# Kernel tuning notes

Hardware: AMD Instinct MI355X
Metric: run time of the kernel (lower is better)

Reference implementation:

```python
import jax, jax.numpy as jnp
import numpy as np


def _skew(p):
    # p: (...,3) -> (...,3,3) skew-symmetric matrices
    x, y, z = p[..., 0], p[..., 1], p[..., 2]
    o = jnp.zeros_like(x)
    return jnp.stack([
        jnp.stack([o, -z, y], -1),
        jnp.stack([z, o, -x], -1),
        jnp.stack([-y, x, o], -1)], -2)


def _so3exp(w):
    # Rodrigues formula for a single (3,) rotation vector
    theta = jnp.linalg.norm(w)
    small = theta < 1e-7
    th = jnp.where(small, 1.0, theta)
    W = _skew(w)
    A = jnp.where(small, 1.0, jnp.sin(th) / th)
    B = jnp.where(small, 0.5, (1.0 - jnp.cos(th)) / (th * th))
    return jnp.eye(3, dtype=w.dtype) + A * W + B * (W @ W)


def setup_inputs() -> dict:
    key = jax.random.key(0)
    k1, k2, k3, k4, k5, k6 = jax.random.split(key, 6)
    N, C, H, W = 100000, 128, 480, 640
    xy = jax.random.uniform(k1, (N, 2), minval=-1.0, maxval=1.0)
    z = jax.random.uniform(k2, (N, 1), minval=4.0, maxval=8.0)
    pts3D = jnp.concatenate([xy, z], -1).astype(jnp.float32)
    feature_ref = jax.random.normal(k3, (N, C), dtype=jnp.float32)
    feature_map_query = jax.random.normal(k4, (C, H, W), dtype=jnp.float32)
    feature_grad_x = jax.random.normal(k5, (C, H, W), dtype=jnp.float32) * 0.1
    feature_grad_y = jax.random.normal(k6, (C, H, W), dtype=jnp.float32) * 0.1
    K = jnp.array([[400.0, 0.0, 320.0], [0.0, 400.0, 200.0], [0.0, 0.0, 1.0]], dtype=jnp.float32)
    return {"pts3D": pts3D, "feature_ref": feature_ref,
            "feature_map_query": feature_map_query,
            "feature_grad_x": feature_grad_x, "feature_grad_y": feature_grad_y,
            "K": K, "n_iters": 5}


def reference(pts3D, feature_ref, feature_map_query, feature_grad_x, feature_grad_y, K, n_iters):
    C, H, W = feature_map_query.shape
    N = pts3D.shape[0]

    def gather(fm, ii, jj):
        return fm[:, ii, jj].T  # (N, C)

    def project(Rm, tv):
        p = pts3D @ Rm.T + tv                       # (N,3) points in camera frame
        uv = p @ K.T
        proj = jnp.round(uv[:, :2] / uv[:, 2:3]).astype(jnp.int32) - 1  # (N,2) [x,y]
        ii = jnp.clip(proj[:, 1], 0, H - 1)          # row (flip)
        jj = jnp.clip(proj[:, 0], 0, W - 1)          # col
        return p, ii, jj

    def step(carry, i):
        R, t, lam, lr, prev_cost = carry
        p, ii, jj = project(R, t)
        error = gather(feature_map_query, ii, jj) - feature_ref  # (N,C)
        cost_mean = (0.5 * (error ** 2).sum(-1)).mean()
        prev_cost = jnp.where(i == 0, cost_mean, prev_cost)
        eye = jnp.broadcast_to(jnp.eye(3, dtype=p.dtype), (N, 3, 3))
        J_p_T = jnp.concatenate([eye, -_skew(p)], -1)            # (N,3,6)
        fx, fy = K[0, 0], K[1, 1]
        x, y, z = p[:, 0], p[:, 1], p[:, 2]
        o = jnp.ones_like(z); zz = jnp.zeros_like(z)
        J_px_p = jnp.stack([fx * o, zz, -fx * x / z, zz, fy * o, -fy * y / z], -1)
        J_px_p = J_px_p.reshape(N, 2, 3) / z[:, None, None]       # (N,2,3)
        gx = gather(feature_grad_x, ii, jj)
        gy = gather(feature_grad_y, ii, jj)
        J_f_px = jnp.stack([gx, gy], -1)                          # (N,C,2)
        J = jnp.einsum('ncp,npq,nqk->nck', J_f_px, J_px_p, J_p_T)  # (N,C,6)
        g = jnp.einsum('nck,nc->k', J, error)                     # (6,)
        Hess = jnp.einsum('nci,ncj->ij', J, J)                    # (6,6)
        Hd = Hess + jnp.diag(jnp.diagonal(Hess) + 1e-9) * lam     # LM damping
        delta = -lr * jnp.linalg.solve(Hd, g)
        dt, dw = delta[:3], delta[3:6]
        dR = _so3exp(dw)
        R_new = dR @ R
        t_new = dR @ t + dt
        _, ii2, jj2 = project(R_new, t_new)
        new_error = gather(feature_map_query, ii2, jj2) - feature_ref
        new_cost = (0.5 * (new_error ** 2).sum(-1)).mean()
        worse = new_cost > prev_cost
        lam = jnp.clip(lam * jnp.where(worse, 10.0, 0.1), 1e-6, 1e4)
        lr = jnp.where(worse, jnp.clip(0.1 * lr, 1e-3, 1.0), 0.1)
        R = jnp.where(worse, R, R_new)
        t = jnp.where(worse, t, t_new)
        prev_cost = jnp.where(worse, prev_cost, new_cost)
        return (R, t, lam, lr, prev_cost), None

    R0 = jnp.eye(3, dtype=pts3D.dtype)
    t0 = jnp.array([1.0, 1.0, 0.0], dtype=pts3D.dtype)
    init = (R0, t0, jnp.float32(0.01), jnp.float32(0.1), jnp.float32(0.0))
    (R, t, _, _, _), _ = jax.lax.scan(step, init, jnp.arange(n_iters))
    return R, t
```

## Files before the change

### kernel.cpp

```cpp
#include <hip/hip_runtime.h>

#define NPTS 100000
#define CCH  128
#define HIMG 480
#define WIMG 640
#define HWSZ (HIMG*WIMG)
#define TROW 384

struct State {
  double accA[28];
  double accC[28];
  double accB;
  double prev_cost;
  float R[9];
  float t[3];
  float Rc[9];
  float tc[3];
  float lam;
  float lr;
};

__device__ State g_st;

__device__ __forceinline__ float sel6(int k, float a0,float a1,float a2,float a3,float a4,float a5){
  float r = a0;
  r = (k==1)?a1:r; r = (k==2)?a2:r; r = (k==3)?a3:r; r = (k==4)?a4:r; r = (k==5)?a5:r;
  return r;
}

__global__ void k_init(){
  if(threadIdx.x==0){
    for(int i=0;i<28;i++){ g_st.accA[i]=0.0; g_st.accC[i]=0.0; }
    g_st.accB=0.0; g_st.prev_cost=0.0;
    g_st.R[0]=1.f; g_st.R[1]=0.f; g_st.R[2]=0.f;
    g_st.R[3]=0.f; g_st.R[4]=1.f; g_st.R[5]=0.f;
    g_st.R[6]=0.f; g_st.R[7]=0.f; g_st.R[8]=1.f;
    g_st.t[0]=1.f; g_st.t[1]=1.f; g_st.t[2]=0.f;
    g_st.lam=0.01f; g_st.lr=0.1f;
  }
}

#define TIDX(c,p) ((c)*66 + ((p) ^ ((((c)>>5)&3)<<4)))

__global__ __launch_bounds__(256) void k_transpose(
    const float* __restrict__ Q, const float* __restrict__ GX,
    const float* __restrict__ GY, float* __restrict__ T)
{
  __shared__ float tile[128*66];
  const int pbase = blockIdx.x * 64;
  const int t = threadIdx.x;

  for(int m=0;m<3;m++){
    const float* __restrict__ src = (m==0)?Q:((m==1)?GX:GY);
    __syncthreads();
    #pragma unroll
    for(int k=0;k<8;k++){
      const int c = (t>>4) + 16*k;
      const float4 v = *reinterpret_cast<const float4*>(src + (size_t)c*HWSZ + pbase + ((t&15)<<2));
      float* d = &tile[TIDX(c, (t&15)<<2)];
      d[0]=v.x; d[1]=v.y; d[2]=v.z; d[3]=v.w;
    }
    __syncthreads();
    const int p  = t>>2;
    const int cb = (t&3)*32;
    float4* dst = reinterpret_cast<float4*>(T + (size_t)(pbase+p)*TROW + m*128 + cb);
    #pragma unroll
    for(int k=0;k<8;k++){
      float4 v;
      v.x = tile[TIDX(cb+4*k+0, p)];
      v.y = tile[TIDX(cb+4*k+1, p)];
      v.z = tile[TIDX(cb+4*k+2, p)];
      v.w = tile[TIDX(cb+4*k+3, p)];
      dst[k] = v;
    }
  }
}

__global__ __launch_bounds__(256) void k_pass(
    const float* __restrict__ pts, const float* __restrict__ ref,
    const float* __restrict__ T,   const float* __restrict__ Kin, int cand)
{
  __shared__ double wacc[4][28];
  const int lane = threadIdx.x & 63;
  const int wid  = threadIdx.x >> 6;

  const float fx=Kin[0], cx=Kin[2], fy=Kin[4], cy=Kin[5];
  const float* Rp = cand ? g_st.Rc : g_st.R;
  const float* tp = cand ? g_st.tc : g_st.t;
  const float R00=Rp[0],R01=Rp[1],R02=Rp[2];
  const float R10=Rp[3],R11=Rp[4],R12=Rp[5];
  const float R20=Rp[6],R21=Rp[7],R22=Rp[8];
  const float t0=tp[0],t1=tp[1],t2=tp[2];

  int role = 3, ci = 0, cj = 0;
  if(lane < 6){ role = 0; ci = lane; cj = lane; }
  else if(lane < 27){
    role = 1;
    const int tt = lane - 6;
    int i = 5;
    i = (tt < 20) ? 4 : i;
    i = (tt < 18) ? 3 : i;
    i = (tt < 15) ? 2 : i;
    i = (tt < 11) ? 1 : i;
    i = (tt <  6) ? 0 : i;
    const int rs = (i==0)?0:(i==1)?6:(i==2)?11:(i==3)?15:(i==4)?18:20;
    ci = i; cj = i + (tt - rs);
  }
  else if(lane == 27){ role = 2; }

  double acc = 0.0;
  const int c0 = lane*2;
  const int wstride = gridDim.x*4;
  for(int n = blockIdx.x*4 + wid; n < NPTS; n += wstride){
    const float X=pts[3*n], Y=pts[3*n+1], Z=pts[3*n+2];
    const float x = R00*X + R01*Y + R02*Z + t0;
    const float y = R10*X + R11*Y + R12*Z + t1;
    const float z = R20*X + R21*Y + R22*Z + t2;
    const float uu = fx*x + cx*z;
    const float vv = fy*y + cy*z;
    const int pjx = (int)rintf(uu/z) - 1;
    const int pjy = (int)rintf(vv/z) - 1;
    const int jj = pjx<0?0:(pjx>(WIMG-1)?(WIMG-1):pjx);
    const int ii = pjy<0?0:(pjy>(HIMG-1)?(HIMG-1):pjy);
    const int idx = ii*WIMG + jj;

    const float* base = T + (size_t)idx*TROW + c0;
    const float2 qq = *reinterpret_cast<const float2*>(base);
    const float2 gg = *reinterpret_cast<const float2*>(base + 128);
    const float2 hh = *reinterpret_cast<const float2*>(base + 256);
    const float2 rr = *reinterpret_cast<const float2*>(ref + n*CCH + c0);
    const float e0 = qq.x-rr.x, e1 = qq.y-rr.y;

    float see = e0*e0 + e1*e1;
    float sb1 = gg.x*e0 + gg.y*e1;
    float sb2 = hh.x*e0 + hh.y*e1;
    float sa11= gg.x*gg.x + gg.y*gg.y;
    float sa12= gg.x*hh.x + gg.y*hh.y;
    float sa22= hh.x*hh.x + hh.y*hh.y;
    #pragma unroll
    for(int m=1;m<64;m<<=1){
      see += __shfl_xor(see,m);
      sb1 += __shfl_xor(sb1,m);
      sb2 += __shfl_xor(sb2,m);
      sa11+= __shfl_xor(sa11,m);
      sa12+= __shfl_xor(sa12,m);
      sa22+= __shfl_xor(sa22,m);
    }

    const float iz = 1.0f/z;
    const float ux = x*iz, vy = y*iz;
    const float m00=fx*iz, m01=0.f,    m02=-fx*ux*iz, m03=-fx*ux*vy,       m04=fx*(1.f+ux*ux), m05=-fx*vy;
    const float m10=0.f,   m11=fy*iz,  m12=-fy*vy*iz, m13=-fy*(1.f+vy*vy), m14=fy*ux*vy,       m15=fy*ux;

    float contrib;
    if(role==0){
      const float M0=sel6(ci,m00,m01,m02,m03,m04,m05);
      const float M1=sel6(ci,m10,m11,m12,m13,m14,m15);
      contrib = M0*sb1 + M1*sb2;
    } else if(role==1){
      const float M0i=sel6(ci,m00,m01,m02,m03,m04,m05);
      const float M1i=sel6(ci,m10,m11,m12,m13,m14,m15);
      const float M0j=sel6(cj,m00,m01,m02,m03,m04,m05);
      const float M1j=sel6(cj,m10,m11,m12,m13,m14,m15);
      contrib = sa11*(M0i*M0j) + sa12*(M0i*M1j + M1i*M0j) + sa22*(M1i*M1j);
    } else if(role==2){
      contrib = see;
    } else {
      contrib = 0.f;
    }
    acc += (double)contrib;
  }

  if(lane<28) wacc[wid][lane] = acc;
  __syncthreads();
  if(threadIdx.x<28){
    double s = wacc[0][threadIdx.x]+wacc[1][threadIdx.x]+wacc[2][threadIdx.x]+wacc[3][threadIdx.x];
    atomicAdd(cand ? &g_st.accC[threadIdx.x] : &g_st.accA[threadIdx.x], s);
  }
}

__global__ void k_update2(){
  if(threadIdx.x!=0) return;
  const double new_cost = 0.5*g_st.accC[27]/(double)NPTS;
  const bool worse = new_cost > g_st.prev_cost;
  float lam = g_st.lam * (worse?10.0f:0.1f);
  g_st.lam = fminf(fmaxf(lam,1e-6f),10000.0f);
  g_st.lr  = worse ? fminf(fmaxf(0.1f*g_st.lr,0.001f),1.0f) : 0.1f;
  if(!worse){
    for(int i=0;i<28;i++) g_st.accA[i]=g_st.accC[i];
    for(int i=0;i<9;i++) g_st.R[i]=g_st.Rc[i];
    for(int i=0;i<3;i++) g_st.t[i]=g_st.tc[i];
    g_st.prev_cost = new_cost;
  }
  for(int i=0;i<28;i++) g_st.accC[i]=0.0;
}

__global__ __launch_bounds__(256) void k_accum(
    const float* __restrict__ pts, const float* __restrict__ ref,
    const float* __restrict__ Q,   const float* __restrict__ GX,
    const float* __restrict__ GY,  const float* __restrict__ Kin)
{
  __shared__ double wacc[4][28];
  const int lane = threadIdx.x & 63;
  const int wid  = threadIdx.x >> 6;

  const float fx=Kin[0], cx=Kin[2], fy=Kin[4], cy=Kin[5];
  const float R00=g_st.R[0],R01=g_st.R[1],R02=g_st.R[2];
  const float R10=g_st.R[3],R11=g_st.R[4],R12=g_st.R[5];
  const float R20=g_st.R[6],R21=g_st.R[7],R22=g_st.R[8];
  const float t0=g_st.t[0],t1=g_st.t[1],t2=g_st.t[2];

  int role = 3, ci = 0, cj = 0;
  if(lane < 6){ role = 0; ci = lane; cj = lane; }
  else if(lane < 27){
    role = 1;
    const int tt = lane - 6;
    int i = 5;
    i = (tt < 20) ? 4 : i;
    i = (tt < 18) ? 3 : i;
    i = (tt < 15) ? 2 : i;
    i = (tt < 11) ? 1 : i;
    i = (tt <  6) ? 0 : i;
    const int rs = (i==0)?0:(i==1)?6:(i==2)?11:(i==3)?15:(i==4)?18:20;
    ci = i; cj = i + (tt - rs);
  }
  else if(lane == 27){ role = 2; }

  double acc = 0.0;
  const int c0 = lane*2;
  const int wstride = gridDim.x*4;
  for(int n = blockIdx.x*4 + wid; n < NPTS; n += wstride){
    const float X=pts[3*n], Y=pts[3*n+1], Z=pts[3*n+2];
    const float x = R00*X + R01*Y + R02*Z + t0;
    const float y = R10*X + R11*Y + R12*Z + t1;
    const float z = R20*X + R21*Y + R22*Z + t2;
    const float uu = fx*x + cx*z;
    const float vv = fy*y + cy*z;
    const int pjx = (int)rintf(uu/z) - 1;
    const int pjy = (int)rintf(vv/z) - 1;
    const int jj = pjx<0?0:(pjx>(WIMG-1)?(WIMG-1):pjx);
    const int ii = pjy<0?0:(pjy>(HIMG-1)?(HIMG-1):pjy);
    const int idx = ii*WIMG + jj;

    const int o0 = c0*HWSZ + idx;
    const float q0 = Q[o0],  q1 = Q[o0+HWSZ];
    const float gx0= GX[o0], gx1= GX[o0+HWSZ];
    const float gy0= GY[o0], gy1= GY[o0+HWSZ];
    const float2 rr = *reinterpret_cast<const float2*>(ref + n*CCH + c0);
    const float e0 = q0-rr.x, e1 = q1-rr.y;

    float see = e0*e0 + e1*e1;
    float sb1 = gx0*e0 + gx1*e1;
    float sb2 = gy0*e0 + gy1*e1;
    float sa11= gx0*gx0 + gx1*gx1;
    float sa12= gx0*gy0 + gx1*gy1;
    float sa22= gy0*gy0 + gy1*gy1;
    #pragma unroll
    for(int m=1;m<64;m<<=1){
      see += __shfl_xor(see,m);
      sb1 += __shfl_xor(sb1,m);
      sb2 += __shfl_xor(sb2,m);
      sa11+= __shfl_xor(sa11,m);
      sa12+= __shfl_xor(sa12,m);
      sa22+= __shfl_xor(sa22,m);
    }

    const float iz = 1.0f/z;
    const float ux = x*iz, vy = y*iz;
    const float m00=fx*iz, m01=0.f,    m02=-fx*ux*iz, m03=-fx*ux*vy,       m04=fx*(1.f+ux*ux), m05=-fx*vy;
    const float m10=0.f,   m11=fy*iz,  m12=-fy*vy*iz, m13=-fy*(1.f+vy*vy), m14=fy*ux*vy,       m15=fy*ux;

    float contrib;
    if(role==0){
      const float M0=sel6(ci,m00,m01,m02,m03,m04,m05);
      const float M1=sel6(ci,m10,m11,m12,m13,m14,m15);
      contrib = M0*sb1 + M1*sb2;
    } else if(role==1){
      const float M0i=sel6(ci,m00,m01,m02,m03,m04,m05);
      const float M1i=sel6(ci,m10,m11,m12,m13,m14,m15);
      const float M0j=sel6(cj,m00,m01,m02,m03,m04,m05);
      const float M1j=sel6(cj,m10,m11,m12,m13,m14,m15);
      contrib = sa11*(M0i*M0j) + sa12*(M0i*M1j + M1i*M0j) + sa22*(M1i*M1j);
    } else if(role==2){
      contrib = see;
    } else {
      contrib = 0.f;
    }
    acc += (double)contrib;
  }

  if(lane<28) wacc[wid][lane] = acc;
  __syncthreads();
  if(threadIdx.x<28){
    double s = wacc[0][threadIdx.x]+wacc[1][threadIdx.x]+wacc[2][threadIdx.x]+wacc[3][threadIdx.x];
    atomicAdd(&g_st.accA[threadIdx.x], s);
  }
}

__global__ __launch_bounds__(256) void k_cost(
    const float* __restrict__ pts, const float* __restrict__ ref,
    const float* __restrict__ Q,   const float* __restrict__ Kin)
{
  __shared__ double wacc[4];
  const int lane = threadIdx.x & 63;
  const int wid  = threadIdx.x >> 6;

  const float fx=Kin[0], cx=Kin[2], fy=Kin[4], cy=Kin[5];
  const float R00=g_st.Rc[0],R01=g_st.Rc[1],R02=g_st.Rc[2];
  const float R10=g_st.Rc[3],R11=g_st.Rc[4],R12=g_st.Rc[5];
  const float R20=g_st.Rc[6],R21=g_st.Rc[7],R22=g_st.Rc[8];
  const float t0=g_st.tc[0],t1=g_st.tc[1],t2=g_st.tc[2];

  double acc = 0.0;
  const int c0 = lane*2;
  const int wstride = gridDim.x*4;
  for(int n = blockIdx.x*4 + wid; n < NPTS; n += wstride){
    const float X=pts[3*n], Y=pts[3*n+1], Z=pts[3*n+2];
    const float x = R00*X + R01*Y + R02*Z + t0;
    const float y = R10*X + R11*Y + R12*Z + t1;
    const float z = R20*X + R21*Y + R22*Z + t2;
    const float uu = fx*x + cx*z;
    const float vv = fy*y + cy*z;
    const int pjx = (int)rintf(uu/z) - 1;
    const int pjy = (int)rintf(vv/z) - 1;
    const int jj = pjx<0?0:(pjx>(WIMG-1)?(WIMG-1):pjx);
    const int ii = pjy<0?0:(pjy>(HIMG-1)?(HIMG-1):pjy);
    const int idx = ii*WIMG + jj;

    const int o0 = c0*HWSZ + idx;
    const float q0 = Q[o0], q1 = Q[o0+HWSZ];
    const float2 rr = *reinterpret_cast<const float2*>(ref + n*CCH + c0);
    const float e0 = q0-rr.x, e1 = q1-rr.y;
    float see = e0*e0 + e1*e1;
    #pragma unroll
    for(int m=1;m<64;m<<=1) see += __shfl_xor(see,m);
    if(lane==0) acc += (double)see;
  }
  if(lane==0) wacc[wid]=acc;
  __syncthreads();
  if(threadIdx.x==0) atomicAdd(&g_st.accB, wacc[0]+wacc[1]+wacc[2]+wacc[3]);
}

__global__ void k_solve(int iter){
  if(threadIdx.x!=0) return;
  const double cost_mean = 0.5*g_st.accA[27]/(double)NPTS;
  if(iter==0) g_st.prev_cost = cost_mean;
  const double lam = (double)g_st.lam;

  double Hm[6][6];
  int m=0;
  for(int i=0;i<6;i++) for(int j=i;j<6;j++){ double v=g_st.accA[6+m]; m++; Hm[i][j]=v; Hm[j][i]=v; }
  double A[6][7];
  for(int i=0;i<6;i++){
    for(int j=0;j<6;j++) A[i][j]=Hm[i][j];
    A[i][i] = Hm[i][i] + lam*(Hm[i][i]+1e-9);
    A[i][6] = g_st.accA[i];
  }
  for(int k=0;k<6;k++){
    int piv=k; double mx=fabs(A[k][k]);
    for(int r=k+1;r<6;r++){ double v=fabs(A[r][k]); if(v>mx){mx=v;piv=r;} }
    if(piv!=k){ for(int c=k;c<7;c++){ double tmp=A[k][c]; A[k][c]=A[piv][c]; A[piv][c]=tmp; } }
    const double inv = 1.0/A[k][k];
    for(int r=k+1;r<6;r++){
      const double f = A[r][k]*inv;
      for(int c=k;c<7;c++) A[r][c] -= f*A[k][c];
    }
  }
  double xsol[6];
  for(int r=5;r>=0;r--){
    double s=A[r][6];
    for(int c=r+1;c<6;c++) s -= A[r][c]*xsol[c];
    xsol[r]=s/A[r][r];
  }
  const double lr = (double)g_st.lr;
  float d[6];
  for(int k=0;k<6;k++) d[k] = (float)(-lr*xsol[k]);

  const float wx=d[3], wy=d[4], wz=d[5];
  const float th2 = wx*wx+wy*wy+wz*wz;
  const float theta = sqrtf(th2);
  const bool small = theta < 1e-7f;
  const float th = small?1.0f:theta;
  const float Aa = small?1.0f:(sinf(th)/th);
  const float Bb = small?0.5f:((1.0f-cosf(th))/(th*th));
  float Wm[3][3] = {{0.f,-wz,wy},{wz,0.f,-wx},{-wy,wx,0.f}};
  float W2[3][3];
  for(int i=0;i<3;i++) for(int j=0;j<3;j++)
    W2[i][j] = Wm[i][0]*Wm[0][j] + Wm[i][1]*Wm[1][j] + Wm[i][2]*Wm[2][j];
  float dR[3][3];
  for(int i=0;i<3;i++) for(int j=0;j<3;j++)
    dR[i][j] = (i==j?1.f:0.f) + Aa*Wm[i][j] + Bb*W2[i][j];

  float Rn[9], tn[3];
  for(int i=0;i<3;i++){
    for(int j=0;j<3;j++)
      Rn[i*3+j] = dR[i][0]*g_st.R[0*3+j] + dR[i][1]*g_st.R[1*3+j] + dR[i][2]*g_st.R[2*3+j];
    tn[i] = dR[i][0]*g_st.t[0] + dR[i][1]*g_st.t[1] + dR[i][2]*g_st.t[2] + d[i];
  }
  for(int i=0;i<9;i++) g_st.Rc[i]=Rn[i];
  for(int i=0;i<3;i++) g_st.tc[i]=tn[i];
  g_st.accB = 0.0;
}

__global__ void k_update(){
  if(threadIdx.x!=0) return;
  const double new_cost = 0.5*g_st.accB/(double)NPTS;
  const bool worse = new_cost > g_st.prev_cost;
  float lam = g_st.lam * (worse?10.0f:0.1f);
  lam = fminf(fmaxf(lam,1e-6f),10000.0f);
  g_st.lam = lam;
  g_st.lr  = worse ? fminf(fmaxf(0.1f*g_st.lr,0.001f),1.0f) : 0.1f;
  if(!worse){
    for(int i=0;i<9;i++) g_st.R[i]=g_st.Rc[i];
    for(int i=0;i<3;i++) g_st.t[i]=g_st.tc[i];
    g_st.prev_cost = new_cost;
  }
  for(int i=0;i<28;i++) g_st.accA[i]=0.0;
}

__global__ void k_write(float* __restrict__ out, int out_size){
  const int i = threadIdx.x;
  if(i<9 && i<out_size) out[i]=g_st.R[i];
  else if(i<12 && i<out_size) out[i]=g_st.t[i-9];
}

extern "C" void kernel_launch(void* const* d_in, const int* in_sizes, int n_in,
                              void* d_out, int out_size, void* d_ws, size_t ws_size,
                              hipStream_t stream) {
  const float* pts = (const float*)d_in[0];
  const float* ref = (const float*)d_in[1];
  const float* Q   = (const float*)d_in[2];
  const float* GX  = (const float*)d_in[3];
  const float* GY  = (const float*)d_in[4];
  const float* Km  = (const float*)d_in[5];
  float* out = (float*)d_out;

  const size_t need = (size_t)HWSZ * TROW * sizeof(float);
  const int GRID = 2048;

  if(d_ws != nullptr && ws_size >= need){
    float* T = (float*)d_ws;
    k_init<<<1,64,0,stream>>>();
    k_transpose<<<HWSZ/64,256,0,stream>>>(Q,GX,GY,T);
    k_pass<<<GRID,256,0,stream>>>(pts,ref,T,Km,0);
    for(int i=0;i<5;i++){
      k_solve<<<1,64,0,stream>>>(i);
      k_pass<<<GRID,256,0,stream>>>(pts,ref,T,Km,1);
      k_update2<<<1,64,0,stream>>>();
    }
    k_write<<<1,64,0,stream>>>(out,out_size);
  } else {
    k_init<<<1,64,0,stream>>>();
    for(int i=0;i<5;i++){
      k_accum<<<GRID,256,0,stream>>>(pts,ref,Q,GX,GY,Km);
      k_solve<<<1,64,0,stream>>>(i);
      k_cost<<<GRID,256,0,stream>>>(pts,ref,Q,Km);
      k_update<<<1,64,0,stream>>>();
    }
    k_write<<<1,64,0,stream>>>(out,out_size);
  }
}
```

Measured before the change: 1.020 ms.

## Restructure LM pipeline: per-lane accumulation, slotted atomics, fused step kernels, finer transpose

Each lane now accumulates all 28 gradient/Hessian/cost terms in registers over its channel pair, and the per-point cross-lane shuffle reductions are replaced by one reduction per block at the end. Block partial sums are spread over 8 atomic slots to reduce contention. The init, solve and update kernels are merged into k_step and k_finish, which removes several tiny launches. The transpose is split into smaller one-map-per-block tiles for more parallelism. The cost is higher register pressure from the 28-entry accumulator and more per-point FMAs per lane.

After: 998.0 us. 1.02x faster.

```diff
diff --git a/kernel.cpp b/kernel.cpp
--- a/kernel.cpp
+++ b/kernel.cpp
@@ -6,10 +6,12 @@
 #define WIMG 640
 #define HWSZ (HIMG*WIMG)
 #define TROW 384
+#define NSLOT 8
 
 struct State {
+  double slotsA[NSLOT][28];
+  double slotsC[NSLOT][28];
   double accA[28];
-  double accC[28];
   double accB;
   double prev_cost;
   float R[9];
@@ -22,57 +24,60 @@
 
 __device__ State g_st;
 
+#define HIDX(i,j) (6 + (6*(i)) - ((i)*((i)-1))/2 + ((j)-(i)))
+
 __device__ __forceinline__ float sel6(int k, float a0,float a1,float a2,float a3,float a4,float a5){
   float r = a0;
   r = (k==1)?a1:r; r = (k==2)?a2:r; r = (k==3)?a3:r; r = (k==4)?a4:r; r = (k==5)?a5:r;
   return r;
 }
 
-__global__ void k_init(){
-  if(threadIdx.x==0){
-    for(int i=0;i<28;i++){ g_st.accA[i]=0.0; g_st.accC[i]=0.0; }
-    g_st.accB=0.0; g_st.prev_cost=0.0;
+#define TP_PIX 32
+#define NTILE (HWSZ/TP_PIX)
+#define TIX(p,c) ((p)*132 + ((c) ^ ((((p)>>2)&3)<<3)))
+
+__global__ __launch_bounds__(256) void k_transpose(
+    const float* __restrict__ Q, const float* __restrict__ GX,
+    const float* __restrict__ GY, float* __restrict__ T)
+{
+  if(blockIdx.x==0 && threadIdx.x==0){
+    for(int s=0;s<NSLOT;s++) for(int k=0;k<28;k++){ g_st.slotsA[s][k]=0.0; g_st.slotsC[s][k]=0.0; }
+    g_st.prev_cost=0.0;
     g_st.R[0]=1.f; g_st.R[1]=0.f; g_st.R[2]=0.f;
     g_st.R[3]=0.f; g_st.R[4]=1.f; g_st.R[5]=0.f;
     g_st.R[6]=0.f; g_st.R[7]=0.f; g_st.R[8]=1.f;
     g_st.t[0]=1.f; g_st.t[1]=1.f; g_st.t[2]=0.f;
     g_st.lam=0.01f; g_st.lr=0.1f;
   }
-}
-
-#define TIDX(c,p) ((c)*66 + ((p) ^ ((((c)>>5)&3)<<4)))
-
-__global__ __launch_bounds__(256) void k_transpose(
-    const float* __restrict__ Q, const float* __restrict__ GX,
-    const float* __restrict__ GY, float* __restrict__ T)
-{
-  __shared__ float tile[128*66];
-  const int pbase = blockIdx.x * 64;
+
+  __shared__ float tile[TP_PIX*132];
+  const int bid = blockIdx.x;
+  const int m   = bid / NTILE;
+  const int tl  = bid - m*NTILE;
+  const int pbase = tl*TP_PIX;
+  const float* __restrict__ src = (m==0)?Q:((m==1)?GX:GY);
   const int t = threadIdx.x;
 
-  for(int m=0;m<3;m++){
-    const float* __restrict__ src = (m==0)?Q:((m==1)?GX:GY);
-    __syncthreads();
-    #pragma unroll
-    for(int k=0;k<8;k++){
-      const int c = (t>>4) + 16*k;
-      const float4 v = *reinterpret_cast<const float4*>(src + (size_t)c*HWSZ + pbase + ((t&15)<<2));
-      float* d = &tile[TIDX(c, (t&15)<<2)];
-      d[0]=v.x; d[1]=v.y; d[2]=v.z; d[3]=v.w;
-    }
-    __syncthreads();
-    const int p  = t>>2;
-    const int cb = (t&3)*32;
-    float4* dst = reinterpret_cast<float4*>(T + (size_t)(pbase+p)*TROW + m*128 + cb);
-    #pragma unroll
-    for(int k=0;k<8;k++){
-      float4 v;
-      v.x = tile[TIDX(cb+4*k+0, p)];
-      v.y = tile[TIDX(cb+4*k+1, p)];
-      v.z = tile[TIDX(cb+4*k+2, p)];
-      v.w = tile[TIDX(cb+4*k+3, p)];
-      dst[k] = v;
-    }
+  const int c_lo = t>>3;
+  const int p4   = (t&7)<<2;
+  #pragma unroll
+  for(int k=0;k<4;k++){
+    const int c = c_lo + 32*k;
+    const float4 v = *reinterpret_cast<const float4*>(src + (size_t)c*HWSZ + pbase + p4);
+    tile[TIX(p4+0,c)] = v.x;
+    tile[TIX(p4+1,c)] = v.y;
+    tile[TIX(p4+2,c)] = v.z;
+    tile[TIX(p4+3,c)] = v.w;
+  }
+  __syncthreads();
+  const int p = t>>3;
+  const int a = t&7;
+  float* dstp = T + (size_t)(pbase+p)*TROW + m*128;
+  #pragma unroll
+  for(int q=0;q<4;q++){
+    const int ch = a*4 + 32*q;
+    const float4 v = *reinterpret_cast<const float4*>(&tile[TIX(p,ch)]);
+    *reinterpret_cast<float4*>(dstp + ch) = v;
   }
 }
 
@@ -91,6 +96,202 @@
   const float R10=Rp[3],R11=Rp[4],R12=Rp[5];
   const float R20=Rp[6],R21=Rp[7],R22=Rp[8];
   const float t0=tp[0],t1=tp[1],t2=tp[2];
+
+  float a[28];
+  #pragma unroll
+  for(int k=0;k<28;k++) a[k]=0.f;
+
+  const int c0 = lane*2;
+  const int wstride = gridDim.x*4;
+  for(int n = blockIdx.x*4 + wid; n < NPTS; n += wstride){
+    const float X=pts[3*n], Y=pts[3*n+1], Z=pts[3*n+2];
+    const float x = R00*X + R01*Y + R02*Z + t0;
+    const float y = R10*X + R11*Y + R12*Z + t1;
+    const float z = R20*X + R21*Y + R22*Z + t2;
+    const float uu = fx*x + cx*z;
+    const float vv = fy*y + cy*z;
+    const int pjx = (int)rintf(uu/z) - 1;
+    const int pjy = (int)rintf(vv/z) - 1;
+    const int jj = pjx<0?0:(pjx>(WIMG-1)?(WIMG-1):pjx);
+    const int ii = pjy<0?0:(pjy>(HIMG-1)?(HIMG-1):pjy);
+    const int idx = ii*WIMG + jj;
+
+    const float* base = T + (size_t)idx*TROW + c0;
+    const float2 qq = *reinterpret_cast<const float2*>(base);
+    const float2 gg = *reinterpret_cast<const float2*>(base + 128);
+    const float2 hh = *reinterpret_cast<const float2*>(base + 256);
+    const float2 rr = *reinterpret_cast<const float2*>(ref + n*CCH + c0);
+    const float e0 = qq.x-rr.x, e1 = qq.y-rr.y;
+
+    const float see = e0*e0 + e1*e1;
+    const float sb1 = gg.x*e0 + gg.y*e1;
+    const float sb2 = hh.x*e0 + hh.y*e1;
+    const float sa11= gg.x*gg.x + gg.y*gg.y;
+    const float sa12= gg.x*hh.x + gg.y*hh.y;
+    const float sa22= hh.x*hh.x + hh.y*hh.y;
+
+    const float iz = 1.0f/z;
+    const float ux = x*iz, vy = y*iz;
+    float M0[6], M1[6];
+    M0[0]=fx*iz; M0[1]=0.f;   M0[2]=-fx*ux*iz; M0[3]=-fx*ux*vy;       M0[4]=fx*(1.f+ux*ux); M0[5]=-fx*vy;
+    M1[0]=0.f;   M1[1]=fy*iz; M1[2]=-fy*vy*iz; M1[3]=-fy*(1.f+vy*vy); M1[4]=fy*ux*vy;       M1[5]=fy*ux;
+
+    #pragma unroll
+    for(int i=0;i<6;i++) a[i] += M0[i]*sb1 + M1[i]*sb2;
+    #pragma unroll
+    for(int i=0;i<6;i++){
+      #pragma unroll
+      for(int j=i;j<6;j++){
+        a[HIDX(i,j)] += sa11*(M0[i]*M0[j]) + sa12*(M0[i]*M1[j]+M1[i]*M0[j]) + sa22*(M1[i]*M1[j]);
+      }
+    }
+    a[27] += see;
+  }
+
+  #pragma unroll
+  for(int k=0;k<28;k++){
+    double v = (double)a[k];
+    #pragma unroll
+    for(int m=1;m<64;m<<=1) v += __shfl_xor(v,m);
+    if(lane==0) wacc[wid][k]=v;
+  }
+  __syncthreads();
+  if(threadIdx.x<28){
+    double s = wacc[0][threadIdx.x]+wacc[1][threadIdx.x]+wacc[2][threadIdx.x]+wacc[3][threadIdx.x];
+    double* slot = cand ? g_st.slotsC[blockIdx.x & (NSLOT-1)] : g_st.slotsA[blockIdx.x & (NSLOT-1)];
+    atomicAdd(&slot[threadIdx.x], s);
+  }
+}
+
+__global__ void k_step(int iter){
+  __shared__ double red[28];
+  __shared__ double sC[28];
+  const int t = threadIdx.x;
+  if(t<28){
+    double c=0.0, aa=0.0;
+    for(int s=0;s<NSLOT;s++){ c += g_st.slotsC[s][t]; aa += g_st.slotsA[s][t]; }
+    sC[t]=c; red[t]=aa;
+  }
+  __syncthreads();
+  if(t!=0) return;
+
+  if(iter>0){
+    const double new_cost = 0.5*sC[27]/(double)NPTS;
+    const bool worse = new_cost > g_st.prev_cost;
+    float lam = g_st.lam * (worse?10.0f:0.1f);
+    g_st.lam = fminf(fmaxf(lam,1e-6f),10000.0f);
+    g_st.lr  = worse ? fminf(fmaxf(0.1f*g_st.lr,0.001f),1.0f) : 0.1f;
+    if(!worse){
+      for(int k=0;k<28;k++){
+        red[k]=sC[k];
+        g_st.slotsA[0][k]=sC[k];
+        for(int s=1;s<NSLOT;s++) g_st.slotsA[s][k]=0.0;
+      }
+      for(int i=0;i<9;i++) g_st.R[i]=g_st.Rc[i];
+      for(int i=0;i<3;i++) g_st.t[i]=g_st.tc[i];
+      g_st.prev_cost = new_cost;
+    }
+    for(int s=0;s<NSLOT;s++) for(int k=0;k<28;k++) g_st.slotsC[s][k]=0.0;
+  } else {
+    g_st.prev_cost = 0.5*red[27]/(double)NPTS;
+  }
+
+  const double lam = (double)g_st.lam;
+  double Hm[6][6];
+  int m=0;
+  for(int i=0;i<6;i++) for(int j=i;j<6;j++){ double v=red[6+m]; m++; Hm[i][j]=v; Hm[j][i]=v; }
+  double A[6][7];
+  for(int i=0;i<6;i++){
+    for(int j=0;j<6;j++) A[i][j]=Hm[i][j];
+    A[i][i] = Hm[i][i] + lam*(Hm[i][i]+1e-9);
+    A[i][6] = red[i];
+  }
+  for(int k=0;k<6;k++){
+    int piv=k; double mx=fabs(A[k][k]);
+    for(int r=k+1;r<6;r++){ double v=fabs(A[r][k]); if(v>mx){mx=v;piv=r;} }
+    if(piv!=k){ for(int c=k;c<7;c++){ double tmp=A[k][c]; A[k][c]=A[piv][c]; A[piv][c]=tmp; } }
+    const double inv = 1.0/A[k][k];
+    for(int r=k+1;r<6;r++){
+      const double f = A[r][k]*inv;
+      for(int c=k;c<7;c++) A[r][c] -= f*A[k][c];
+    }
+  }
+  double xsol[6];
+  for(int r=5;r>=0;r--){
+    double s=A[r][6];
+    for(int c=r+1;c<6;c++) s -= A[r][c]*xsol[c];
+    xsol[r]=s/A[r][r];
+  }
+  const double lr = (double)g_st.lr;
+  float d[6];
+  for(int k=0;k<6;k++) d[k] = (float)(-lr*xsol[k]);
+
+  const float wx=d[3], wy=d[4], wz=d[5];
+  const float th2 = wx*wx+wy*wy+wz*wz;
+  const float theta = sqrtf(th2);
+  const bool small = theta < 1e-7f;
+  const float th = small?1.0f:theta;
+  const float Aa = small?1.0f:(sinf(th)/th);
+  const float Bb = small?0.5f:((1.0f-cosf(th))/(th*th));
+  float Wm[3][3] = {{0.f,-wz,wy},{wz,0.f,-wx},{-wy,wx,0.f}};
+  float W2[3][3];
+  for(int i=0;i<3;i++) for(int j=0;j<3;j++)
+    W2[i][j] = Wm[i][0]*Wm[0][j] + Wm[i][1]*Wm[1][j] + Wm[i][2]*Wm[2][j];
+  float dR[3][3];
+  for(int i=0;i<3;i++) for(int j=0;j<3;j++)
+    dR[i][j] = (i==j?1.f:0.f) + Aa*Wm[i][j] + Bb*W2[i][j];
+
+  float Rn[9], tn[3];
+  for(int i=0;i<3;i++){
+    for(int j=0;j<3;j++)
+      Rn[i*3+j] = dR[i][0]*g_st.R[0*3+j] + dR[i][1]*g_st.R[1*3+j] + dR[i][2]*g_st.R[2*3+j];
+    tn[i] = dR[i][0]*g_st.t[0] + dR[i][1]*g_st.t[1] + dR[i][2]*g_st.t[2] + d[i];
+  }
+  for(int i=0;i<9;i++) g_st.Rc[i]=Rn[i];
+  for(int i=0;i<3;i++) g_st.tc[i]=tn[i];
+}
+
+__global__ void k_finish(float* __restrict__ out, int out_size){
+  const int t = threadIdx.x;
+  if(t==0){
+    double c=0.0; for(int s=0;s<NSLOT;s++) c += g_st.slotsC[s][27];
+    const double new_cost = 0.5*c/(double)NPTS;
+    if(!(new_cost > g_st.prev_cost)){
+      for(int i=0;i<9;i++) g_st.R[i]=g_st.Rc[i];
+      for(int i=0;i<3;i++) g_st.t[i]=g_st.tc[i];
+    }
+  }
+  __syncthreads();
+  if(t<9 && t<out_size) out[t]=g_st.R[t];
+  else if(t<12 && t<out_size) out[t]=g_st.t[t-9];
+}
+
+__global__ void k_init(){
+  if(threadIdx.x==0){
+    for(int i=0;i<28;i++) g_st.accA[i]=0.0;
+    g_st.accB=0.0; g_st.prev_cost=0.0;
+    g_st.R[0]=1.f; g_st.R[1]=0.f; g_st.R[2]=0.f;
+    g_st.R[3]=0.f; g_st.R[4]=1.f; g_st.R[5]=0.f;
+    g_st.R[6]=0.f; g_st.R[7]=0.f; g_st.R[8]=1.f;
+    g_st.t[0]=1.f; g_st.t[1]=1.f; g_st.t[2]=0.f;
+    g_st.lam=0.01f; g_st.lr=0.1f;
+  }
+}
+
+__global__ __launch_bounds__(256) void k_accum(
+    const float* __restrict__ pts, const float* __restrict__ ref,
+    const float* __restrict__ Q,   const float* __restrict__ GX,
+    const float* __restrict__ GY,  const float* __restrict__ Kin)
+{
+  __shared__ double wacc[4][28];
+  const int lane = threadIdx.x & 63;
+  const int wid  = threadIdx.x >> 6;
+
+  const float fx=Kin[0], cx=Kin[2], fy=Kin[4], cy=Kin[5];
+  const float R00=g_st.R[0],R01=g_st.R[1],R02=g_st.R[2];
+  const float R10=g_st.R[3],R11=g_st.R[4],R12=g_st.R[5];
+  const float R20=g_st.R[6],R21=g_st.R[7],R22=g_st.R[8];
+  const float t0=g_st.t[0],t1=g_st.t[1],t2=g_st.t[2];
 
   int role = 3, ci = 0, cj = 0;
   if(lane < 6){ role = 0; ci = lane; cj = lane; }
@@ -124,19 +325,19 @@
     const int ii = pjy<0?0:(pjy>(HIMG-1)?(HIMG-1):pjy);
     const int idx = ii*WIMG + jj;
 
-    const float* base = T + (size_t)idx*TROW + c0;
-    const float2 qq = *reinterpret_cast<const float2*>(base);
-    const float2 gg = *reinterpret_cast<const float2*>(base + 128);
-    const float2 hh = *reinterpret_cast<const float2*>(base + 256);
+    const int o0 = c0*HWSZ + idx;
+    const float q0 = Q[o0],  q1 = Q[o0+HWSZ];
+    const float gx0= GX[o0], gx1= GX[o0+HWSZ];
+    const float gy0= GY[o0], gy1= GY[o0+HWSZ];
     const float2 rr = *reinterpret_cast<const float2*>(ref + n*CCH + c0);
-    const float e0 = qq.x-rr.x, e1 = qq.y-rr.y;
+    const float e0 = q0-rr.x, e1 = q1-rr.y;
 
     float see = e0*e0 + e1*e1;
-    float sb1 = gg.x*e0 + gg.y*e1;
-    float sb2 = hh.x*e0 + hh.y*e1;
-    float sa11= gg.x*gg.x + gg.y*gg.y;
-    float sa12= gg.x*hh.x + gg.y*hh.y;
-    float sa22= hh.x*hh.x + hh.y*hh.y;
+    float sb1 = gx0*e0 + gx1*e1;
+    float sb2 = gy0*e0 + gy1*e1;
+    float sa11= gx0*gx0 + gx1*gx1;
+    float sa12= gx0*gy0 + gx1*gy1;
+    float sa22= gy0*gy0 + gy1*gy1;
     #pragma unroll
     for(int m=1;m<64;m<<=1){
       see += __shfl_xor(see,m);
@@ -175,56 +376,23 @@
   __syncthreads();
   if(threadIdx.x<28){
     double s = wacc[0][threadIdx.x]+wacc[1][threadIdx.x]+wacc[2][threadIdx.x]+wacc[3][threadIdx.x];
-    atomicAdd(cand ? &g_st.accC[threadIdx.x] : &g_st.accA[threadIdx.x], s);
-  }
-}
-
-__global__ void k_update2(){
-  if(threadIdx.x!=0) return;
-  const double new_cost = 0.5*g_st.accC[27]/(double)NPTS;
-  const bool worse = new_cost > g_st.prev_cost;
-  float lam = g_st.lam * (worse?10.0f:0.1f);
-  g_st.lam = fminf(fmaxf(lam,1e-6f),10000.0f);
-  g_st.lr  = worse ? fminf(fmaxf(0.1f*g_st.lr,0.001f),1.0f) : 0.1f;
-  if(!worse){
-    for(int i=0;i<28;i++) g_st.accA[i]=g_st.accC[i];
-    for(int i=0;i<9;i++) g_st.R[i]=g_st.Rc[i];
-    for(int i=0;i<3;i++) g_st.t[i]=g_st.tc[i];
-    g_st.prev_cost = new_cost;
-  }
-  for(int i=0;i<28;i++) g_st.accC[i]=0.0;
-}
-
-__global__ __launch_bounds__(256) void k_accum(
+    atomicAdd(&g_st.accA[threadIdx.x], s);
+  }
+}
+
+__global__ __launch_bounds__(256) void k_cost(
     const float* __restrict__ pts, const float* __restrict__ ref,
-    const float* __restrict__ Q,   const float* __restrict__ GX,
-    const float* __restrict__ GY,  const float* __restrict__ Kin)
+    const float* __restrict__ Q,   const float* __restrict__ Kin)
 {
-  __shared__ double wacc[4][28];
+  __shared__ double wacc[4];
   const int lane = threadIdx.x & 63;
   const int wid  = threadIdx.x >> 6;
 
   const float fx=Kin[0], cx=Kin[2], fy=Kin[4], cy=Kin[5];
-  const float R00=g_st.R[0],R01=g_st.R[1],R02=g_st.R[2];
-  const float R10=g_st.R[3],R11=g_st.R[4],R12=g_st.R[5];
-  const float R20=g_st.R[6],R21=g_st.R[7],R22=g_st.R[8];
-  const float t0=g_st.t[0],t1=g_st.t[1],t2=g_st.t[2];
-
-  int role = 3, ci = 0, cj = 0;
-  if(lane < 6){ role = 0; ci = lane; cj = lane; }
-  else if(lane < 27){
-    role = 1;
-    const int tt = lane - 6;
-    int i = 5;
-    i = (tt < 20) ? 4 : i;
-    i = (tt < 18) ? 3 : i;
-    i = (tt < 15) ? 2 : i;
-    i = (tt < 11) ? 1 : i;
-    i = (tt <  6) ? 0 : i;
-    const int rs = (i==0)?0:(i==1)?6:(i==2)?11:(i==3)?15:(i==4)?18:20;
-    ci = i; cj = i + (tt - rs);
-  }
-  else if(lane == 27){ role = 2; }
+  const float R00=g_st.Rc[0],R01=g_st.Rc[1],R02=g_st.Rc[2];
+  const float R10=g_st.Rc[3],R11=g_st.Rc[4],R12=g_st.Rc[5];
+  const float R20=g_st.Rc[6],R21=g_st.Rc[7],R22=g_st.Rc[8];
+  const float t0=g_st.tc[0],t1=g_st.tc[1],t2=g_st.tc[2];
 
   double acc = 0.0;
   const int c0 = lane*2;
@@ -243,91 +411,6 @@
     const int idx = ii*WIMG + jj;
 
     const int o0 = c0*HWSZ + idx;
-    const float q0 = Q[o0],  q1 = Q[o0+HWSZ];
-    const float gx0= GX[o0], gx1= GX[o0+HWSZ];
-    const float gy0= GY[o0], gy1= GY[o0+HWSZ];
-    const float2 rr = *reinterpret_cast<const float2*>(ref + n*CCH + c0);
-    const float e0 = q0-rr.x, e1 = q1-rr.y;
-
-    float see = e0*e0 + e1*e1;
-    float sb1 = gx0*e0 + gx1*e1;
-    float sb2 = gy0*e0 + gy1*e1;
-    float sa11= gx0*gx0 + gx1*gx1;
-    float sa12= gx0*gy0 + gx1*gy1;
-    float sa22= gy0*gy0 + gy1*gy1;
-    #pragma unroll
-    for(int m=1;m<64;m<<=1){
-      see += __shfl_xor(see,m);
-      sb1 += __shfl_xor(sb1,m);
-      sb2 += __shfl_xor(sb2,m);
-      sa11+= __shfl_xor(sa11,m);
-      sa12+= __shfl_xor(sa12,m);
-      sa22+= __shfl_xor(sa22,m);
-    }
-
-    const float iz = 1.0f/z;
-    const float ux = x*iz, vy = y*iz;
-    const float m00=fx*iz, m01=0.f,    m02=-fx*ux*iz, m03=-fx*ux*vy,       m04=fx*(1.f+ux*ux), m05=-fx*vy;
-    const float m10=0.f,   m11=fy*iz,  m12=-fy*vy*iz, m13=-fy*(1.f+vy*vy), m14=fy*ux*vy,       m15=fy*ux;
-
-    float contrib;
-    if(role==0){
-      const float M0=sel6(ci,m00,m01,m02,m03,m04,m05);
-      const float M1=sel6(ci,m10,m11,m12,m13,m14,m15);
-      contrib = M0*sb1 + M1*sb2;
-    } else if(role==1){
-      const float M0i=sel6(ci,m00,m01,m02,m03,m04,m05);
-      const float M1i=sel6(ci,m10,m11,m12,m13,m14,m15);
-      const float M0j=sel6(cj,m00,m01,m02,m03,m04,m05);
-      const float M1j=sel6(cj,m10,m11,m12,m13,m14,m15);
-      contrib = sa11*(M0i*M0j) + sa12*(M0i*M1j + M1i*M0j) + sa22*(M1i*M1j);
-    } else if(role==2){
-      contrib = see;
-    } else {
-      contrib = 0.f;
-    }
-    acc += (double)contrib;
-  }
-
-  if(lane<28) wacc[wid][lane] = acc;
-  __syncthreads();
-  if(threadIdx.x<28){
-    double s = wacc[0][threadIdx.x]+wacc[1][threadIdx.x]+wacc[2][threadIdx.x]+wacc[3][threadIdx.x];
-    atomicAdd(&g_st.accA[threadIdx.x], s);
-  }
-}
-
-__global__ __launch_bounds__(256) void k_cost(
-    const float* __restrict__ pts, const float* __restrict__ ref,
-    const float* __restrict__ Q,   const float* __restrict__ Kin)
-{
-  __shared__ double wacc[4];
-  const int lane = threadIdx.x & 63;
-  const int wid  = threadIdx.x >> 6;
-
-  const float fx=Kin[0], cx=Kin[2], fy=Kin[4], cy=Kin[5];
-  const float R00=g_st.Rc[0],R01=g_st.Rc[1],R02=g_st.Rc[2];
-  const float R10=g_st.Rc[3],R11=g_st.Rc[4],R12=g_st.Rc[5];
-  const float R20=g_st.Rc[6],R21=g_st.Rc[7],R22=g_st.Rc[8];
-  const float t0=g_st.tc[0],t1=g_st.tc[1],t2=g_st.tc[2];
-
-  double acc = 0.0;
-  const int c0 = lane*2;
-  const int wstride = gridDim.x*4;
-  for(int n = blockIdx.x*4 + wid; n < NPTS; n += wstride){
-    const float X=pts[3*n], Y=pts[3*n+1], Z=pts[3*n+2];
-    const float x = R00*X + R01*Y + R02*Z + t0;
-    const float y = R10*X + R11*Y + R12*Z + t1;
-    const float z = R20*X + R21*Y + R22*Z + t2;
-    const float uu = fx*x + cx*z;
-    const float vv = fy*y + cy*z;
-    const int pjx = (int)rintf(uu/z) - 1;
-    const int pjy = (int)rintf(vv/z) - 1;
-    const int jj = pjx<0?0:(pjx>(WIMG-1)?(WIMG-1):pjx);
-    const int ii = pjy<0?0:(pjy>(HIMG-1)?(HIMG-1):pjy);
-    const int idx = ii*WIMG + jj;
-
-    const int o0 = c0*HWSZ + idx;
     const float q0 = Q[o0], q1 = Q[o0+HWSZ];
     const float2 rr = *reinterpret_cast<const float2*>(ref + n*CCH + c0);
     const float e0 = q0-rr.x, e1 = q1-rr.y;
@@ -440,15 +523,13 @@
 
   if(d_ws != nullptr && ws_size >= need){
     float* T = (float*)d_ws;
-    k_init<<<1,64,0,stream>>>();
-    k_transpose<<<HWSZ/64,256,0,stream>>>(Q,GX,GY,T);
+    k_transpose<<<3*NTILE,256,0,stream>>>(Q,GX,GY,T);
     k_pass<<<GRID,256,0,stream>>>(pts,ref,T,Km,0);
     for(int i=0;i<5;i++){
-      k_solve<<<1,64,0,stream>>>(i);
+      k_step<<<1,64,0,stream>>>(i);
       k_pass<<<GRID,256,0,stream>>>(pts,ref,T,Km,1);
-      k_update2<<<1,64,0,stream>>>();
-    }
-    k_write<<<1,64,0,stream>>>(out,out_size);
+    }
+    k_finish<<<1,64,0,stream>>>(out,out_size);
   } else {
     k_init<<<1,64,0,stream>>>();
     for(int i=0;i<5;i++){
```
